# Optimization experiments

Hardware: AMD Instinct MI355X
Metric: run time of the kernel (lower is better)

Reference implementation:

```python
import jax, jax.numpy as jnp
import numpy as np

EMBED, ACT, DETER, STOCH, HID = 1536, 10, 2048, 64, 1024
T, B = 64, 256
LN_EPS = 1e-3


def _ln(x, s, b):
    mu = jnp.mean(x, axis=-1, keepdims=True)
    var = jnp.mean(jnp.square(x - mu), axis=-1, keepdims=True)
    return (x - mu) * jax.lax.rsqrt(var + LN_EPS) * s + b


def setup_inputs() -> dict:
    key = jax.random.key(0)
    ks = jax.random.split(key, 20)
    g = lambda k, shp, fan: jax.random.normal(k, shp, jnp.float32) * (1.0 / np.sqrt(fan))
    inp = {
        "embeds": jax.random.normal(ks[0], (T, B, EMBED), jnp.float32),
        "actions": jax.random.normal(ks[1], (T, B, ACT), jnp.float32),
        "h_t": jnp.zeros((B, DETER), jnp.float32),
        "z_t": jnp.zeros((B, STOCH), jnp.float32),
        "noise": jax.random.normal(ks[2], (T, B, STOCH), jnp.float32),
        # DeterNext
        "z_mlp_w": g(ks[3], (HID // 2, STOCH), STOCH),
        "z_mlp_b": jnp.zeros((HID // 2,), jnp.float32),
        "a_mlp_w": g(ks[4], (HID // 2, ACT), ACT),  # bias=False
        "ln_za_s": jnp.ones((HID,), jnp.float32),
        "ln_za_b": jnp.zeros((HID,), jnp.float32),
        # GRUCell (torch layout: [3*deter, in])
        "gru_wih": g(ks[5], (3 * DETER, HID), HID),
        "gru_whh": g(ks[6], (3 * DETER, DETER), DETER),
        "gru_bih": jnp.zeros((3 * DETER,), jnp.float32),
        "gru_bhh": jnp.zeros((3 * DETER,), jnp.float32),
        # PosteriorNext
        "post_h_w": g(ks[7], (HID, DETER), DETER),
        "post_h_b": jnp.zeros((HID,), jnp.float32),
        "post_e_w": g(ks[8], (HID, EMBED), EMBED),
        "post_e_b": jnp.zeros((HID,), jnp.float32),
        "ln_post_s": jnp.ones((HID,), jnp.float32),
        "ln_post_b": jnp.zeros((HID,), jnp.float32),
        "post_w": g(ks[9], (2 * STOCH, HID), HID),
        "post_b": jnp.zeros((2 * STOCH,), jnp.float32),
        # PriorNext
        "prior_h_w": g(ks[10], (HID, DETER), DETER),
        "prior_h_b": jnp.zeros((HID,), jnp.float32),
        "ln_prior_s": jnp.ones((HID,), jnp.float32),
        "ln_prior_b": jnp.zeros((HID,), jnp.float32),
        "prior_w": g(ks[11], (2 * STOCH, HID), HID),
        "prior_b": jnp.zeros((2 * STOCH,), jnp.float32),
    }
    return inp


def _rssm_forward(embeds, actions, h0, z0, noise,
                  z_mlp_w, z_mlp_b, a_mlp_w, ln_za_s, ln_za_b,
                  gru_wih, gru_whh, gru_bih, gru_bhh,
                  post_h_w, post_h_b, post_e_w, post_e_b, ln_post_s, ln_post_b,
                  post_w, post_b,
                  prior_h_w, prior_h_b, ln_prior_s, ln_prior_b, prior_w, prior_b):
    def step(carry, xs):
        h, z = carry
        e, a, n = xs
        # DeterNext: concat(z_mlp(z), a_mlp(a)) -> LN -> ELU
        x = jnp.concatenate([z @ z_mlp_w.T + z_mlp_b, a @ a_mlp_w.T], axis=-1)
        za = jax.nn.elu(_ln(x, ln_za_s, ln_za_b))
        # GRUCell
        gi = za @ gru_wih.T + gru_bih
        gh = h @ gru_whh.T + gru_bhh
        ir, iu, ic = jnp.split(gi, 3, axis=-1)
        hr, hu, hc = jnp.split(gh, 3, axis=-1)
        r = jax.nn.sigmoid(ir + hr)
        u = jax.nn.sigmoid(iu + hu)
        c = jnp.tanh(ic + r * hc)
        h1 = (1.0 - u) * c + u * h
        # PosteriorNext
        p = jax.nn.elu(_ln(h1 @ post_h_w.T + post_h_b + e @ post_e_w.T + post_e_b,
                           ln_post_s, ln_post_b))
        post = p @ post_w.T + post_b  # [B, 2*stoch]
        mean, sraw = jnp.split(post, 2, axis=-1)
        std = 2.0 * jax.nn.sigmoid(sraw) + 0.1
        z1 = mean + std * n  # rsample with externally-supplied noise
        return (h1, z1), (post, h1, z1)

    (_, _), (posts, states_h, post_z_samples) = jax.lax.scan(
        step, (h0, z0), (embeds, actions, noise))
    # batch prior over all timesteps
    pr = jax.nn.elu(_ln(states_h @ prior_h_w.T + prior_h_b, ln_prior_s, ln_prior_b))
    priors = pr @ prior_w.T + prior_b  # [T, B, 2*stoch]
    features = jnp.concatenate([states_h, post_z_samples], axis=-1)  # [T,B,deter+stoch]
    return priors, posts, post_z_samples, features


def reference(embeds, actions, h_t, z_t, noise,
              z_mlp_w, z_mlp_b, a_mlp_w, ln_za_s, ln_za_b,
              gru_wih, gru_whh, gru_bih, gru_bhh,
              post_h_w, post_h_b, post_e_w, post_e_b, ln_post_s, ln_post_b,
              post_w, post_b,
              prior_h_w, prior_h_b, ln_prior_s, ln_prior_b, prior_w, prior_b):
    return _rssm_forward(embeds, actions, h_t, z_t, noise,
                         z_mlp_w, z_mlp_b, a_mlp_w, ln_za_s, ln_za_b,
                         gru_wih, gru_whh, gru_bih, gru_bhh,
                         post_h_w, post_h_b, post_e_w, post_e_b, ln_post_s, ln_post_b,
                         post_w, post_b,
                         prior_h_w, prior_h_b, ln_prior_s, ln_prior_b, prior_w, prior_b)
```

## Files before the change

kernel.cpp:

```cpp
#include <hip/hip_runtime.h>

#define LN_EPS 1e-3f

typedef short s8v __attribute__((ext_vector_type(8)));
typedef float f4v __attribute__((ext_vector_type(4)));
typedef unsigned short u16;

__device__ __forceinline__ u16 f2bf(float f) {
  unsigned int x = __float_as_uint(f);
  x += 0x7fffu + ((x >> 16) & 1u);
  return (u16)(x >> 16);
}
__device__ __forceinline__ float bf2f(u16 u) {
  return __uint_as_float(((unsigned int)u) << 16);
}

__device__ __forceinline__ void glds16(const u16* g, void* l) {
  __builtin_amdgcn_global_load_lds(
      (const __attribute__((address_space(1))) void*)g,
      (__attribute__((address_space(3))) void*)l, 16, 0, 0);
}

__global__ void k_cvt(const float* __restrict__ src, u16* __restrict__ dst, int n) {
  int i = blockIdx.x * blockDim.x + threadIdx.x;
  int stride = gridDim.x * blockDim.x;
  for (; i < n; i += stride) dst[i] = f2bf(src[i]);
}

__global__ void k_packgru(const float* __restrict__ wih,
                          const float* __restrict__ whh, u16* __restrict__ wt) {
  int u = blockIdx.x * 256 + threadIdx.x;
  int nt = u / 73728;
  int r1 = u % 73728;
  int s = r1 / 1536;
  int r2 = r1 % 1536;
  int sub = r2 / 512;
  int r3 = r2 % 512;
  int ch = r3 / 64;
  int row = r3 % 64;
  int j = nt * 64 + row;
  int kbase = s * 64 + ch * 8;
  s8v v;
#pragma unroll
  for (int e = 0; e < 8; ++e) {
    int kk = kbase + e;
    float x;
    if (sub == 0) {
      x = kk < 1024 ? wih[(size_t)j * 1024 + kk] : whh[(size_t)j * 2048 + kk - 1024];
    } else if (sub == 1) {
      int jj = 2048 + j;
      x = kk < 1024 ? wih[(size_t)jj * 1024 + kk] : whh[(size_t)jj * 2048 + kk - 1024];
    } else {
      int jj = 4096 + j;
      x = (s < 16) ? wih[(size_t)jj * 1024 + kk] : whh[(size_t)jj * 2048 + kk - 1024];
    }
    v[e] = (short)f2bf(x);
  }
  *(s8v*)(wt + (size_t)u * 8) = v;
}

__global__ void k_packB(const float* __restrict__ src, u16* __restrict__ dst,
                        int K, int BN, int total) {
  int u = blockIdx.x * 256 + threadIdx.x;
  if (u >= total) return;
  int ns = K >> 6;
  int perNt = ns * 8 * BN;
  int nt = u / perNt;
  int r1 = u % perNt;
  int s = r1 / (8 * BN);
  int r2 = r1 % (8 * BN);
  int ch = r2 / BN;
  int row = r2 % BN;
  int j = nt * BN + row;
  int k = s * 64 + ch * 8;
  const float* sp = src + (size_t)j * K + k;
  s8v v;
#pragma unroll
  for (int e = 0; e < 8; ++e) v[e] = (short)f2bf(sp[e]);
  *(s8v*)(dst + (size_t)u * 8) = v;
}

__global__ void k_hinit(const float* __restrict__ h0, float* __restrict__ hf,
                        u16* __restrict__ acat) {
  int i = blockIdx.x * 256 + threadIdx.x;
  int b = i >> 11, j = i & 2047;
  float v = h0[i];
  hf[i] = v;
  acat[(size_t)b * 3072 + 1024 + j] = f2bf(v);
}

__global__ __launch_bounds__(256) void k_za(
    const float* __restrict__ zsrc, const float* __restrict__ act,
    const float* __restrict__ zw, const float* __restrict__ zb,
    const float* __restrict__ aw, const float* __restrict__ lns,
    const float* __restrict__ lnb, u16* __restrict__ acat) {
  const int b = blockIdx.x, tid = threadIdx.x;
  __shared__ float zsh[64];
  __shared__ float ash[12];
  __shared__ float wred[8];
  if (tid < 64) zsh[tid] = zsrc[b * 64 + tid];
  if (tid < 10) ash[tid] = act[b * 10 + tid];
  __syncthreads();
  float x[4];
#pragma unroll
  for (int i = 0; i < 2; ++i) {
    int c = tid + i * 256;
    const float4* wp = (const float4*)(zw + c * 64);
    float a = zb[c];
#pragma unroll
    for (int k = 0; k < 16; ++k) {
      float4 v = wp[k];
      a += zsh[k * 4] * v.x + zsh[k * 4 + 1] * v.y + zsh[k * 4 + 2] * v.z +
           zsh[k * 4 + 3] * v.w;
    }
    x[i] = a;
  }
#pragma unroll
  for (int i = 2; i < 4; ++i) {
    int c2 = tid + (i - 2) * 256;
    const float* wp = aw + c2 * 10;
    float a = 0.f;
#pragma unroll
    for (int k = 0; k < 10; ++k) a += ash[k] * wp[k];
    x[i] = a;
  }
  float s = x[0] + x[1] + x[2] + x[3];
#pragma unroll
  for (int o = 1; o < 64; o <<= 1) s += __shfl_xor(s, o);
  if ((tid & 63) == 0) wred[tid >> 6] = s;
  __syncthreads();
  float mu = (wred[0] + wred[1] + wred[2] + wred[3]) * (1.f / 1024.f);
  float q = 0.f;
#pragma unroll
  for (int i = 0; i < 4; ++i) {
    float d = x[i] - mu;
    q += d * d;
  }
#pragma unroll
  for (int o = 1; o < 64; o <<= 1) q += __shfl_xor(q, o);
  if ((tid & 63) == 0) wred[4 + (tid >> 6)] = q;
  __syncthreads();
  float rs = rsqrtf((wred[4] + wred[5] + wred[6] + wred[7]) * (1.f / 1024.f) + LN_EPS);
  int cols[4] = {tid, tid + 256, 512 + tid, 768 + tid};
#pragma unroll
  for (int i = 0; i < 4; ++i) {
    int c = cols[i];
    float y = (x[i] - mu) * rs * lns[c] + lnb[c];
    y = y > 0.f ? y : expm1f(y);
    acat[(size_t)b * 3072 + c] = f2bf(y);
  }
}

__global__ __launch_bounds__(256) void k_gru(
    const u16* __restrict__ acat_r, const u16* __restrict__ wt,
    const float* __restrict__ bih, const float* __restrict__ bhh,
    const float* __restrict__ hf_r, float* __restrict__ hf_w,
    u16* __restrict__ acat_w, float* __restrict__ feat, int t) {
  const int hw = blockIdx.x;
  const int logical = (hw & 7) * 32 + (hw >> 3);
  const int mg = logical & 7;
  const int nt = logical >> 3;
  const int m0 = mg * 32;
  const int tid = threadIdx.x;
  const int lane = tid & 63;
  const int w = tid >> 6;
  const int lr = lane & 15, lk = lane >> 4;

  __shared__ __align__(16) char smem[2][28672];

  const int arow = 8 * w + (lane >> 3);
  const int acol8 = ((lane & 7) ^ (arow & 7)) * 8;
  const u16* aSrc = acat_r + (size_t)(m0 + arow) * 3072 + acol8;
  const u16* wtNt = wt + (size_t)nt * 48 * 3 * 4096;

  f4v accr[2], accu[2], acci[2], acch[2];
  accr[0] = accr[1] = accu[0] = accu[1] = (f4v)(0.f);
  acci[0] = acci[1] = acch[0] = acch[1] = (f4v)(0.f);

#define K1_STAGE(BB, S) { \
    char* base = &smem[BB][0]; \
    glds16(aSrc + (S) * 64, base + w * 1024); \
    const u16* bsrc = wtNt + (size_t)(S) * 3 * 4096; \
    _Pragma("unroll") for (int i = 0; i < 6; ++i) { \
      int cf = w + i * 4; \
      glds16(bsrc + (cf * 64 + lane) * 8, base + 4096 + cf * 1024); \
    } }

#define K1_COMP(BB, ACCX) { \
    char* base = &smem[BB][0]; \
    _Pragma("unroll") for (int kk = 0; kk < 2; ++kk) { \
      int ch = kk * 4 + lk; \
      int r0 = lr, r1 = 16 + lr; \
      s8v a0 = *(const s8v*)(base + r0 * 128 + ((ch ^ (r0 & 7)) * 16)); \
      s8v a1 = *(const s8v*)(base + r1 * 128 + ((ch ^ (r1 & 7)) * 16)); \
      int rb = (w * 16 + lr) * 16; \
      s8v br = *(const s8v*)(base + 4096 + ch * 1024 + rb); \
      s8v bu = *(const s8v*)(base + 12288 + ch * 1024 + rb); \
      s8v bx = *(const s8v*)(base + 20480 + ch * 1024 + rb); \
      accr[0] = __builtin_amdgcn_mfma_f32_16x16x32_bf16(a0, br, accr[0], 0, 0, 0); \
      accr[1] = __builtin_amdgcn_mfma_f32_16x16x32_bf16(a1, br, accr[1], 0, 0, 0); \
      accu[0] = __builtin_amdgcn_mfma_f32_16x16x32_bf16(a0, bu, accu[0], 0, 0, 0); \
      accu[1] = __builtin_amdgcn_mfma_f32_16x16x32_bf16(a1, bu, accu[1], 0, 0, 0); \
      ACCX[0] = __builtin_amdgcn_mfma_f32_16x16x32_bf16(a0, bx, ACCX[0], 0, 0, 0); \
      ACCX[1] = __builtin_amdgcn_mfma_f32_16x16x32_bf16(a1, bx, ACCX[1], 0, 0, 0); \
    } }

  K1_STAGE(0, 0)
  int buf = 0;
  for (int s = 0; s < 16; ++s) {
    asm volatile("s_waitcnt vmcnt(0)" ::: "memory");
    __builtin_amdgcn_s_barrier();
    __builtin_amdgcn_sched_barrier(0);
    K1_STAGE(buf ^ 1, s + 1)
    K1_COMP(buf, acci)
    buf ^= 1;
  }
  for (int s = 16; s < 48; ++s) {
    asm volatile("s_waitcnt vmcnt(0)" ::: "memory");
    __builtin_amdgcn_s_barrier();
    __builtin_amdgcn_sched_barrier(0);
    if (s + 1 < 48) K1_STAGE(buf ^ 1, s + 1)
    K1_COMP(buf, acch)
    buf ^= 1;
  }

  const int j = nt * 64 + w * 16 + lr;
  const float b_ri = bih[j], b_rh = bhh[j];
  const float b_ui = bih[2048 + j], b_uh = bhh[2048 + j];
  const float b_ci = bih[4096 + j], b_ch = bhh[4096 + j];
#pragma unroll
  for (int m = 0; m < 2; ++m) {
#pragma unroll
    for (int r = 0; r < 4; ++r) {
      int grow = m0 + m * 16 + lk * 4 + r;
      float vr = accr[m][r] + b_ri + b_rh;
      float vu = accu[m][r] + b_ui + b_uh;
      float ic = acci[m][r] + b_ci;
      float hc = acch[m][r] + b_ch;
      float rg = 1.f / (1.f + expf(-vr));
      float ug = 1.f / (1.f + expf(-vu));
      float c = tanhf(ic + rg * hc);
      float hold = hf_r[(size_t)grow * 2048 + j];
      float h1 = (1.f - ug) * c + ug * hold;
      hf_w[(size_t)grow * 2048 + j] = h1;
      acat_w[(size_t)grow * 3072 + 1024 + j] = f2bf(h1);
      feat[(size_t)(t * 256 + grow) * 2112 + j] = h1;
    }
  }
#undef K1_STAGE
#undef K1_COMP
}

__global__ __launch_bounds__(256) void k_post(
    const u16* __restrict__ acat_h, const u16* __restrict__ wp,
    const float* __restrict__ bias, const u16* __restrict__ epart_t,
    float* __restrict__ xbuf) {
  const int bx = blockIdx.x;
  const int mg = bx & 7, nt = bx >> 3;
  const int m0 = mg * 32;
  const int tid = threadIdx.x;
  const int lane = tid & 63;
  const int w = tid >> 6;
  const int lr = lane & 15, lk = lane >> 4;

  __shared__ __align__(16) char smem[2][12288];

  const int arow = 8 * w + (lane >> 3);
  const int acol8 = ((lane & 7) ^ (arow & 7)) * 8;
  const u16* aSrc = acat_h + (size_t)(m0 + arow) * 3072 + 1024 + acol8;
  const u16* wpNt = wp + (size_t)nt * 32 * 4096;

  f4v acc[2];
  acc[0] = (f4v)(0.f);
  acc[1] = (f4v)(0.f);

#define K2_STAGE(BB, S) { \
    char* base = &smem[BB][0]; \
    glds16(aSrc + (S) * 64, base + w * 1024); \
    const u16* bsrc = wpNt + (size_t)(S) * 4096; \
    _Pragma("unroll") for (int i = 0; i < 2; ++i) { \
      int cf = w + i * 4; \
      glds16(bsrc + (cf * 64 + lane) * 8, base + 4096 + cf * 1024); \
    } }

  K2_STAGE(0, 0)
  int buf = 0;
  for (int s = 0; s < 32; ++s) {
    asm volatile("s_waitcnt vmcnt(0)" ::: "memory");
    __builtin_amdgcn_s_barrier();
    __builtin_amdgcn_sched_barrier(0);
    if (s + 1 < 32) K2_STAGE(buf ^ 1, s + 1)
    char* base = &smem[buf][0];
#pragma unroll
    for (int kk = 0; kk < 2; ++kk) {
      int ch = kk * 4 + lk;
      int r0 = lr, r1 = 16 + lr;
      s8v a0 = *(const s8v*)(base + r0 * 128 + ((ch ^ (r0 & 7)) * 16));
      s8v a1 = *(const s8v*)(base + r1 * 128 + ((ch ^ (r1 & 7)) * 16));
      s8v b = *(const s8v*)(base + 4096 + ch * 1024 + (w * 16 + lr) * 16);
      acc[0] = __builtin_amdgcn_mfma_f32_16x16x32_bf16(a0, b, acc[0], 0, 0, 0);
      acc[1] = __builtin_amdgcn_mfma_f32_16x16x32_bf16(a1, b, acc[1], 0, 0, 0);
    }
    buf ^= 1;
  }
  const int col = nt * 64 + w * 16 + lr;
#pragma unroll
  for (int m = 0; m < 2; ++m) {
#pragma unroll
    for (int r = 0; r < 4; ++r) {
      int grow = m0 + m * 16 + lk * 4 + r;
      float v = acc[m][r] + bias[col] + bf2f(epart_t[(size_t)grow * 1024 + col]);
      xbuf[(size_t)grow * 1024 + col] = v;
    }
  }
#undef K2_STAGE
}

__global__ __launch_bounds__(512) void k_postz(
    const float* __restrict__ xb, const u16* __restrict__ pw,
    const float* __restrict__ lns, const float* __restrict__ lnb,
    const float* __restrict__ pb, float* __restrict__ posts_t,
    const float* __restrict__ noise_t, float* __restrict__ zout,
    float* __restrict__ feat, int t) {
  const int m0 = blockIdx.x * 32;
  const int tid = threadIdx.x;
  const int lane = tid & 63;
  const int w = tid >> 6;
  const int lr = lane & 15, lk = lane >> 4;
  __shared__ __align__(16) u16 As[2][32][64];
  __shared__ __align__(16) u16 Bs[2][8][128][8];
  __shared__ float lmu[32], lrs[32];
  __shared__ float ps[32][132];
  {
    int row = tid >> 4, sg = tid & 15;
    const float4* xp = (const float4*)(xb + (size_t)(m0 + row) * 1024 + sg * 64);
    float s = 0.f, q = 0.f;
#pragma unroll
    for (int i = 0; i < 16; ++i) {
      float4 v = xp[i];
      s += v.x + v.y + v.z + v.w;
      q += v.x * v.x + v.y * v.y + v.z * v.z + v.w * v.w;
    }
#pragma unroll
    for (int o = 1; o < 16; o <<= 1) {
      s += __shfl_xor(s, o);
      q += __shfl_xor(q, o);
    }
    if (sg == 0) {
      float mu = s * (1.f / 1024.f);
      lmu[row] = mu;
      lrs[row] = rsqrtf(q * (1.f / 1024.f) - mu * mu + LN_EPS);
    }
  }
  __syncthreads();

#define K3_STAGEA(BB, S) if (tid < 256) { \
    int row = tid >> 3, k8 = tid & 7; \
    const float* xp = xb + (size_t)(m0 + row) * 1024 + (S) * 64 + k8 * 8; \
    float mu = lmu[row], rs = lrs[row]; \
    s8v v; \
    _Pragma("unroll") for (int e = 0; e < 8; ++e) { \
      int c = (S) * 64 + k8 * 8 + e; \
      float y = (xp[e] - mu) * rs * lns[c] + lnb[c]; \
      y = y > 0.f ? y : expm1f(y); \
      v[e] = (short)f2bf(y); \
    } \
    *(s8v*)((char*)&As[BB][0][0] + row * 128 + ((k8 ^ (row & 7)) * 16)) = v; }

#define K3_STAGEB(BB, S) { \
    const u16* bsrc = pw + (size_t)(S) * 8192; \
    glds16(bsrc + (((w >> 1) * 128 + (w & 1) * 64 + lane) * 8), \
           (char*)&Bs[BB][0][0][0] + w * 1024); \
    glds16(bsrc + ((((w >> 1) + 4) * 128 + (w & 1) * 64 + lane) * 8), \
           (char*)&Bs[BB][0][0][0] + w * 1024 + 8192); }

  f4v acc[2];
  acc[0] = (f4v)(0.f);
  acc[1] = (f4v)(0.f);
  K3_STAGEA(0, 0)
  K3_STAGEB(0, 0)
  __syncthreads();
  int buf = 0;
  for (int s = 0; s < 16; ++s) {
    if (s + 1 < 16) {
      K3_STAGEA(buf ^ 1, s + 1)
      K3_STAGEB(buf ^ 1, s + 1)
    }
#pragma unroll
    for (int kk = 0; kk < 2; ++kk) {
      int ch = kk * 4 + lk;
      int r0 = lr, r1 = 16 + lr;
      s8v a0 = *(const s8v*)((char*)&As[buf][0][0] + r0 * 128 + ((ch ^ (r0 & 7)) * 16));
      s8v a1 = *(const s8v*)((char*)&As[buf][0][0] + r1 * 128 + ((ch ^ (r1 & 7)) * 16));
      s8v b = *(const s8v*)((char*)&Bs[buf][0][0][0] + ch * 2048 + (w * 16 + lr) * 16);
      acc[0] = __builtin_amdgcn_mfma_f32_16x16x32_bf16(a0, b, acc[0], 0, 0, 0);
      acc[1] = __builtin_amdgcn_mfma_f32_16x16x32_bf16(a1, b, acc[1], 0, 0, 0);
    }
    __syncthreads();
    buf ^= 1;
  }
#pragma unroll
  for (int m = 0; m < 2; ++m) {
#pragma unroll
    for (int r = 0; r < 4; ++r) {
      int row = m * 16 + lk * 4 + r;
      int col = w * 16 + lr;
      float v = acc[m][r] + pb[col];
      posts_t[(size_t)(m0 + row) * 128 + col] = v;
      ps[row][col] = v;
    }
  }
  __syncthreads();
#pragma unroll
  for (int q = 0; q < 4; ++q) {
    int e = q * 512 + tid;
    int row = e >> 6, j = e & 63;
    float mean = ps[row][j], sraw = ps[row][64 + j];
    float sd = 2.f / (1.f + expf(-sraw)) + 0.1f;
    float z = mean + sd * noise_t[(m0 + row) * 64 + j];
    zout[(m0 + row) * 64 + j] = z;
    feat[(size_t)(t * 256 + m0 + row) * 2112 + 2048 + j] = z;
  }
#undef K3_STAGEA
#undef K3_STAGEB
}

template <bool AF32, bool OUTBF16>
__global__ __launch_bounds__(512) void k_gemm8(
    const void* __restrict__ Av, int lda, const u16* __restrict__ Bw, int ldb,
    int nstage, float* __restrict__ Cf, u16* __restrict__ Cb, int ldc,
    const float* __restrict__ bias) {
  const int bx = blockIdx.x, by = blockIdx.y;
  const int tid = threadIdx.x;
  const int m0 = bx * 64;
  const int n0 = by * 128;
  __shared__ __align__(16) u16 As[64][72];
  __shared__ __align__(16) u16 Bs[128][72];
  const int lane = tid & 63;
  const int w = tid >> 6;
  const int wr = w >> 2;
  const int wc = w & 3;
  const int lr = lane & 15;
  const int lk = lane >> 4;

  f4v acc[2][2];
#pragma unroll
  for (int m = 0; m < 2; ++m)
#pragma unroll
    for (int n = 0; n < 2; ++n) acc[m][n] = (f4v)(0.0f);

  for (int s = 0; s < nstage; ++s) {
    const int k0 = s << 6;
    {
      int row = tid >> 3, k8 = (tid & 7) << 3;
      if (AF32) {
        const float* ap = (const float*)Av + (size_t)(m0 + row) * lda + k0 + k8;
        float4 f0 = *(const float4*)ap;
        float4 f1 = *(const float4*)(ap + 4);
        s8v v;
        v[0] = (short)f2bf(f0.x); v[1] = (short)f2bf(f0.y);
        v[2] = (short)f2bf(f0.z); v[3] = (short)f2bf(f0.w);
        v[4] = (short)f2bf(f1.x); v[5] = (short)f2bf(f1.y);
        v[6] = (short)f2bf(f1.z); v[7] = (short)f2bf(f1.w);
        *(s8v*)&As[row][k8] = v;
      } else {
        *(s8v*)&As[row][k8] =
            *(const s8v*)((const u16*)Av + (size_t)(m0 + row) * lda + k0 + k8);
      }
    }
#pragma unroll
    for (int it = 0; it < 2; ++it) {
      int c = tid + it * 512;
      int row = c >> 3, k8 = (c & 7) << 3;
      *(s8v*)&Bs[row][k8] = *(const s8v*)(Bw + (size_t)(n0 + row) * ldb + k0 + k8);
    }
    __syncthreads();
#pragma unroll
    for (int kk = 0; kk < 2; ++kk) {
      const int koff = kk * 32 + lk * 8;
      s8v a[2], b[2];
      a[0] = *(const s8v*)&As[wr * 32 + lr][koff];
      a[1] = *(const s8v*)&As[wr * 32 + 16 + lr][koff];
      b[0] = *(const s8v*)&Bs[wc * 32 + lr][koff];
      b[1] = *(const s8v*)&Bs[wc * 32 + 16 + lr][koff];
#pragma unroll
      for (int m = 0; m < 2; ++m)
#pragma unroll
        for (int n = 0; n < 2; ++n)
          acc[m][n] =
              __builtin_amdgcn_mfma_f32_16x16x32_bf16(a[m], b[n], acc[m][n], 0, 0, 0);
    }
    __syncthreads();
  }
#pragma unroll
  for (int m = 0; m < 2; ++m) {
#pragma unroll
    for (int n = 0; n < 2; ++n) {
#pragma unroll
      for (int r = 0; r < 4; ++r) {
        int row = m0 + wr * 32 + m * 16 + lk * 4 + r;
        int col = n0 + wc * 32 + n * 16 + lr;
        float v = acc[m][n][r];
        if (bias) v += bias[col];
        if (OUTBF16)
          Cb[(size_t)row * ldc + col] = f2bf(v);
        else
          Cf[(size_t)row * ldc + col] = v;
      }
    }
  }
}

__global__ __launch_bounds__(256) void k_lnelu(const u16* __restrict__ xsrc,
                                               const float* __restrict__ s,
                                               const float* __restrict__ bb,
                                               u16* __restrict__ out) {
  int row = blockIdx.x, tid = threadIdx.x;
  __shared__ float red[256];
  float v[4];
#pragma unroll
  for (int i = 0; i < 4; ++i) {
    size_t idx = (size_t)row * 1024 + tid + i * 256;
    v[i] = bf2f(xsrc[idx]);
  }
  float sm = v[0] + v[1] + v[2] + v[3];
  red[tid] = sm;
  __syncthreads();
  for (int o = 128; o > 0; o >>= 1) {
    if (tid < o) red[tid] += red[tid + o];
    __syncthreads();
  }
  float mu = red[0] * (1.0f / 1024.0f);
  __syncthreads();
  float q = 0.f;
#pragma unroll
  for (int i = 0; i < 4; ++i) {
    float d = v[i] - mu;
    q += d * d;
  }
  red[tid] = q;
  __syncthreads();
  for (int o = 128; o > 0; o >>= 1) {
    if (tid < o) red[tid] += red[tid + o];
    __syncthreads();
  }
  float rs = rsqrtf(red[0] * (1.0f / 1024.0f) + LN_EPS);
#pragma unroll
  for (int i = 0; i < 4; ++i) {
    int c = tid + i * 256;
    float y = (v[i] - mu) * rs * s[c] + bb[c];
    y = y > 0.f ? y : expm1f(y);
    out[(size_t)row * 1024 + c] = f2bf(y);
  }
}

extern "C" void kernel_launch(void* const* d_in, const int* in_sizes, int n_in,
                              void* d_out, int out_size, void* d_ws,
                              size_t ws_size, hipStream_t stream) {
  const float* embeds = (const float*)d_in[0];
  const float* actions = (const float*)d_in[1];
  const float* h_t = (const float*)d_in[2];
  const float* z_t = (const float*)d_in[3];
  const float* noise = (const float*)d_in[4];
  const float* z_mlp_w = (const float*)d_in[5];
  const float* z_mlp_b = (const float*)d_in[6];
  const float* a_mlp_w = (const float*)d_in[7];
  const float* ln_za_s = (const float*)d_in[8];
  const float* ln_za_b = (const float*)d_in[9];
  const float* gru_wih = (const float*)d_in[10];
  const float* gru_whh = (const float*)d_in[11];
  const float* gru_bih = (const float*)d_in[12];
  const float* gru_bhh = (const float*)d_in[13];
  const float* post_h_w = (const float*)d_in[14];
  const float* post_h_b = (const float*)d_in[15];
  const float* post_e_w = (const float*)d_in[16];
  const float* post_e_b = (const float*)d_in[17];
  const float* ln_post_s = (const float*)d_in[18];
  const float* ln_post_b = (const float*)d_in[19];
  const float* post_w = (const float*)d_in[20];
  const float* post_b = (const float*)d_in[21];
  const float* prior_h_w = (const float*)d_in[22];
  const float* prior_h_b = (const float*)d_in[23];
  const float* ln_prior_s = (const float*)d_in[24];
  const float* ln_prior_b = (const float*)d_in[25];
  const float* prior_w = (const float*)d_in[26];
  const float* prior_b = (const float*)d_in[27];

  float* out = (float*)d_out;
  float* out_priors = out;
  float* out_posts = out + 2097152;
  float* out_z = out + 4194304;
  float* out_feat = out + 5242880;

  char* ws = (char*)d_ws;
  size_t off = 0;
  auto alloc = [&](size_t bytes) {
    char* p = ws + off;
    off += (bytes + 255) & ~(size_t)255;
    return p;
  };
  char* regW = alloc((size_t)32 * 48 * 3 * 4096 * 2);
  u16* wt = (u16*)regW;
  u16* prx_b = (u16*)regW;
  u16* posthP = (u16*)alloc((size_t)1024 * 2048 * 2);
  u16* postwP = (u16*)alloc((size_t)128 * 1024 * 2);
  u16* poste_b = (u16*)alloc((size_t)1024 * 1536 * 2);
  u16* priorh_b = (u16*)alloc((size_t)1024 * 2048 * 2);
  u16* priorw_b = (u16*)alloc((size_t)128 * 1024 * 2);
  u16* acat0 = (u16*)alloc((size_t)256 * 3072 * 2);
  u16* acat1 = (u16*)alloc((size_t)256 * 3072 * 2);
  float* hf0 = (float*)alloc((size_t)256 * 2048 * 4);
  float* hf1 = (float*)alloc((size_t)256 * 2048 * 4);
  float* xbuf = (float*)alloc((size_t)256 * 1024 * 4);
  char* regU = alloc((size_t)16384 * 1024 * 2);
  u16* e_part = (u16*)regU;
  u16* p_pr = (u16*)regU;

  u16* acat[2] = {acat0, acat1};
  float* hf[2] = {hf0, hf1};

  k_packgru<<<9216, 256, 0, stream>>>(gru_wih, gru_whh, wt);
  k_packB<<<1024, 256, 0, stream>>>(post_h_w, posthP, 2048, 64, 262144);
  k_packB<<<64, 256, 0, stream>>>(post_w, postwP, 1024, 128, 16384);
  k_cvt<<<512, 256, 0, stream>>>(post_e_w, poste_b, 1024 * 1536);
  k_cvt<<<512, 256, 0, stream>>>(prior_h_w, priorh_b, 1024 * 2048);
  k_cvt<<<64, 256, 0, stream>>>(prior_w, priorw_b, 128 * 1024);
  k_hinit<<<2048, 256, 0, stream>>>(h_t, hf0, acat0);

  k_gemm8<true, true><<<dim3(256, 8), 512, 0, stream>>>(
      embeds, 1536, poste_b, 1536, 24, nullptr, e_part, 1024, post_e_b);

  for (int t = 0; t < 64; ++t) {
    const int rI = t & 1, wI = rI ^ 1;
    const float* zsrc = (t == 0) ? z_t : (out_z + (size_t)(t - 1) * 16384);
    k_za<<<256, 256, 0, stream>>>(zsrc, actions + (size_t)t * 2560, z_mlp_w,
                                  z_mlp_b, a_mlp_w, ln_za_s, ln_za_b, acat[rI]);
    k_gru<<<256, 256, 0, stream>>>(acat[rI], wt, gru_bih, gru_bhh, hf[rI],
                                   hf[wI], acat[wI], out_feat, t);
    k_post<<<128, 256, 0, stream>>>(acat[wI], posthP, post_h_b,
                                    e_part + (size_t)t * 262144, xbuf);
    k_postz<<<8, 512, 0, stream>>>(xbuf, postwP, ln_post_s, ln_post_b, post_b,
                                   out_posts + (size_t)t * 32768,
                                   noise + (size_t)t * 16384,
                                   out_z + (size_t)t * 16384, out_feat, t);
  }

  k_gemm8<true, true><<<dim3(256, 8), 512, 0, stream>>>(
      out_feat, 2112, priorh_b, 2048, 32, nullptr, prx_b, 1024, prior_h_b);
  k_lnelu<<<16384, 256, 0, stream>>>(prx_b, ln_prior_s, ln_prior_b, p_pr);
  k_gemm8<false, false><<<dim3(256, 1), 512, 0, stream>>>(
      p_pr, 1024, priorw_b, 1024, 16, out_priors, nullptr, 128, prior_b);
}
```

Before: 7.119 ms.

## Fuse next-step z/action MLP into postz and retile GRU with triple buffering

Moves the per-step z/action MLP plus layernorm into the tail of k_postz, where it runs on the next timestep's action, so one launch per step disappears. The z MLP runs on MFMA using packed weights, and the action weights are pre-transposed. The GRU kernel now uses 512-thread blocks with 64-row tiles on a 128-block grid, and a 3-stage async load pipeline with partial vmcnt waits. k_post and k_postz get the same prefetch-before-wait pipelining; the tradeoffs are a large LDS footprint in postz, fewer GRU blocks, and extra serial work on only 8 blocks.

```diff
diff --git a/kernel.cpp b/kernel.cpp
--- a/kernel.cpp
+++ b/kernel.cpp
@@ -5,6 +5,8 @@
 typedef short s8v __attribute__((ext_vector_type(8)));
 typedef float f4v __attribute__((ext_vector_type(4)));
 typedef unsigned short u16;
+
+#define MFMA16 __builtin_amdgcn_mfma_f32_16x16x32_bf16
 
 __device__ __forceinline__ u16 f2bf(float f) {
   unsigned int x = __float_as_uint(f);
@@ -20,6 +22,8 @@
       (const __attribute__((address_space(1))) void*)g,
       (__attribute__((address_space(3))) void*)l, 16, 0, 0);
 }
+
+#define RAW_BAR() do { __builtin_amdgcn_s_barrier(); __builtin_amdgcn_sched_barrier(0); } while (0)
 
 __global__ void k_cvt(const float* __restrict__ src, u16* __restrict__ dst, int n) {
   int i = blockIdx.x * blockDim.x + threadIdx.x;
@@ -80,20 +84,26 @@
   *(s8v*)(dst + (size_t)u * 8) = v;
 }
 
+__global__ void k_trA(const float* __restrict__ aw, float* __restrict__ awT) {
+  int i = blockIdx.x * 256 + threadIdx.x;
+  if (i >= 5120) return;
+  int k = i >> 9, c = i & 511;
+  awT[i] = aw[c * 10 + k];
+}
+
 __global__ void k_hinit(const float* __restrict__ h0, float* __restrict__ hf,
-                        u16* __restrict__ acat) {
+                        u16* __restrict__ hcat) {
   int i = blockIdx.x * 256 + threadIdx.x;
-  int b = i >> 11, j = i & 2047;
   float v = h0[i];
   hf[i] = v;
-  acat[(size_t)b * 3072 + 1024 + j] = f2bf(v);
-}
-
-__global__ __launch_bounds__(256) void k_za(
+  hcat[i] = f2bf(v);
+}
+
+__global__ __launch_bounds__(256) void k_za0(
     const float* __restrict__ zsrc, const float* __restrict__ act,
     const float* __restrict__ zw, const float* __restrict__ zb,
     const float* __restrict__ aw, const float* __restrict__ lns,
-    const float* __restrict__ lnb, u16* __restrict__ acat) {
+    const float* __restrict__ lnb, u16* __restrict__ za) {
   const int b = blockIdx.x, tid = threadIdx.x;
   __shared__ float zsh[64];
   __shared__ float ash[12];
@@ -147,127 +157,128 @@
     int c = cols[i];
     float y = (x[i] - mu) * rs * lns[c] + lnb[c];
     y = y > 0.f ? y : expm1f(y);
-    acat[(size_t)b * 3072 + c] = f2bf(y);
-  }
-}
-
-__global__ __launch_bounds__(256) void k_gru(
-    const u16* __restrict__ acat_r, const u16* __restrict__ wt,
-    const float* __restrict__ bih, const float* __restrict__ bhh,
-    const float* __restrict__ hf_r, float* __restrict__ hf_w,
-    u16* __restrict__ acat_w, float* __restrict__ feat, int t) {
+    za[(size_t)b * 1024 + c] = f2bf(y);
+  }
+}
+
+__global__ __launch_bounds__(512) void k_gru(
+    const u16* __restrict__ za, const u16* __restrict__ hcat_r,
+    const u16* __restrict__ wt, const float* __restrict__ bih,
+    const float* __restrict__ bhh, const float* __restrict__ hf_r,
+    float* __restrict__ hf_w, u16* __restrict__ hcat_w,
+    float* __restrict__ feat, int t) {
   const int hw = blockIdx.x;
-  const int logical = (hw & 7) * 32 + (hw >> 3);
-  const int mg = logical & 7;
-  const int nt = logical >> 3;
+  const int logical = (hw & 7) * 16 + (hw >> 3);
+  const int mg = logical & 3;
+  const int nt = logical >> 2;
+  const int m0 = mg * 64;
+  const int tid = threadIdx.x;
+  const int lane = tid & 63;
+  const int w = tid >> 6;
+  const int lr = lane & 15, lk = lane >> 4;
+  const int mh = w & 1, cq = w >> 1;
+
+  __shared__ __align__(16) char bufs[3][32768];
+
+  const int arow = w * 8 + (lane >> 3);
+  const int acol8 = ((lane & 7) ^ (arow & 7)) * 8;
+  const u16* aZ = za + (size_t)(m0 + arow) * 1024 + acol8;
+  const u16* aH = hcat_r + (size_t)(m0 + arow) * 2048 + acol8;
+  const u16* wtNt = wt + (size_t)nt * 48 * 12288;
+
+  f4v accr0 = (f4v)(0.f), accr1 = (f4v)(0.f);
+  f4v accu0 = (f4v)(0.f), accu1 = (f4v)(0.f);
+  f4v acci0 = (f4v)(0.f), acci1 = (f4v)(0.f);
+  f4v acch0 = (f4v)(0.f), acch1 = (f4v)(0.f);
+
+#define G_STAGE(S) { \
+    char* base = &bufs[(S) % 3][0]; \
+    const u16* ap = ((S) < 16) ? (aZ + (S) * 64) : (aH + ((S) - 16) * 64); \
+    glds16(ap, base + w * 1024); \
+    const u16* bsrc = wtNt + (size_t)(S) * 12288; \
+    _Pragma("unroll") for (int jj = 0; jj < 3; ++jj) { \
+      int c = w + jj * 8; \
+      glds16(bsrc + c * 512 + lane * 8, base + 8192 + c * 1024); \
+    } }
+
+#define G_COMP(S, X0, X1) { \
+    char* base = &bufs[(S) % 3][0]; \
+    _Pragma("unroll") for (int kk = 0; kk < 2; ++kk) { \
+      int ch = kk * 4 + lk; \
+      int r0 = mh * 32 + lr, r1 = mh * 32 + 16 + lr; \
+      s8v a0 = *(const s8v*)(base + r0 * 128 + ((ch ^ (r0 & 7)) << 4)); \
+      s8v a1 = *(const s8v*)(base + r1 * 128 + ((ch ^ (r1 & 7)) << 4)); \
+      int boff = 8192 + ch * 1024 + ((cq * 16 + lr) << 4); \
+      s8v br = *(const s8v*)(base + boff); \
+      s8v bu = *(const s8v*)(base + boff + 8192); \
+      s8v bx = *(const s8v*)(base + boff + 16384); \
+      accr0 = MFMA16(a0, br, accr0, 0, 0, 0); \
+      accr1 = MFMA16(a1, br, accr1, 0, 0, 0); \
+      accu0 = MFMA16(a0, bu, accu0, 0, 0, 0); \
+      accu1 = MFMA16(a1, bu, accu1, 0, 0, 0); \
+      X0 = MFMA16(a0, bx, X0, 0, 0, 0); \
+      X1 = MFMA16(a1, bx, X1, 0, 0, 0); \
+    } }
+
+  G_STAGE(0)
+  G_STAGE(1)
+  for (int s = 0; s < 48; ++s) {
+    if (s + 2 < 48) { G_STAGE(s + 2) }
+    if (s < 46) asm volatile("s_waitcnt vmcnt(8)" ::: "memory");
+    else if (s == 46) asm volatile("s_waitcnt vmcnt(4)" ::: "memory");
+    else asm volatile("s_waitcnt vmcnt(0)" ::: "memory");
+    RAW_BAR();
+    if (s < 16) { G_COMP(s, acci0, acci1) }
+    else { G_COMP(s, acch0, acch1) }
+    RAW_BAR();
+  }
+#undef G_STAGE
+#undef G_COMP
+
+  const int col = nt * 64 + cq * 16 + lr;
+  const float b_r = bih[col] + bhh[col];
+  const float b_u = bih[2048 + col] + bhh[2048 + col];
+  const float b_ci = bih[4096 + col];
+  const float b_ch = bhh[4096 + col];
+#define G_EPI(AR, AU, AI, AH, MO) \
+  _Pragma("unroll") for (int r = 0; r < 4; ++r) { \
+    int grow = m0 + mh * 32 + (MO) + lk * 4 + r; \
+    float vr = AR[r] + b_r; \
+    float vu = AU[r] + b_u; \
+    float ic = AI[r] + b_ci; \
+    float hc = AH[r] + b_ch; \
+    float rg = 1.f / (1.f + expf(-vr)); \
+    float ug = 1.f / (1.f + expf(-vu)); \
+    float c = tanhf(ic + rg * hc); \
+    float hold = hf_r[(size_t)grow * 2048 + col]; \
+    float h1 = (1.f - ug) * c + ug * hold; \
+    hf_w[(size_t)grow * 2048 + col] = h1; \
+    hcat_w[(size_t)grow * 2048 + col] = f2bf(h1); \
+    feat[(size_t)(t * 256 + grow) * 2112 + col] = h1; \
+  }
+  G_EPI(accr0, accu0, acci0, acch0, 0)
+  G_EPI(accr1, accu1, acci1, acch1, 16)
+#undef G_EPI
+}
+
+__global__ __launch_bounds__(256) void k_post(
+    const u16* __restrict__ hcat, const u16* __restrict__ wp,
+    const float* __restrict__ bias, const u16* __restrict__ epart_t,
+    float* __restrict__ xbuf) {
+  const int hw = blockIdx.x;
+  const int logical = (hw & 7) * 16 + (hw >> 3);
+  const int mg = logical & 7, nt = logical >> 3;
   const int m0 = mg * 32;
   const int tid = threadIdx.x;
   const int lane = tid & 63;
   const int w = tid >> 6;
   const int lr = lane & 15, lk = lane >> 4;
 
-  __shared__ __align__(16) char smem[2][28672];
+  __shared__ __align__(16) char smem[2][12288];
 
   const int arow = 8 * w + (lane >> 3);
   const int acol8 = ((lane & 7) ^ (arow & 7)) * 8;
-  const u16* aSrc = acat_r + (size_t)(m0 + arow) * 3072 + acol8;
-  const u16* wtNt = wt + (size_t)nt * 48 * 3 * 4096;
-
-  f4v accr[2], accu[2], acci[2], acch[2];
-  accr[0] = accr[1] = accu[0] = accu[1] = (f4v)(0.f);
-  acci[0] = acci[1] = acch[0] = acch[1] = (f4v)(0.f);
-
-#define K1_STAGE(BB, S) { \
-    char* base = &smem[BB][0]; \
-    glds16(aSrc + (S) * 64, base + w * 1024); \
-    const u16* bsrc = wtNt + (size_t)(S) * 3 * 4096; \
-    _Pragma("unroll") for (int i = 0; i < 6; ++i) { \
-      int cf = w + i * 4; \
-      glds16(bsrc + (cf * 64 + lane) * 8, base + 4096 + cf * 1024); \
-    } }
-
-#define K1_COMP(BB, ACCX) { \
-    char* base = &smem[BB][0]; \
-    _Pragma("unroll") for (int kk = 0; kk < 2; ++kk) { \
-      int ch = kk * 4 + lk; \
-      int r0 = lr, r1 = 16 + lr; \
-      s8v a0 = *(const s8v*)(base + r0 * 128 + ((ch ^ (r0 & 7)) * 16)); \
-      s8v a1 = *(const s8v*)(base + r1 * 128 + ((ch ^ (r1 & 7)) * 16)); \
-      int rb = (w * 16 + lr) * 16; \
-      s8v br = *(const s8v*)(base + 4096 + ch * 1024 + rb); \
-      s8v bu = *(const s8v*)(base + 12288 + ch * 1024 + rb); \
-      s8v bx = *(const s8v*)(base + 20480 + ch * 1024 + rb); \
-      accr[0] = __builtin_amdgcn_mfma_f32_16x16x32_bf16(a0, br, accr[0], 0, 0, 0); \
-      accr[1] = __builtin_amdgcn_mfma_f32_16x16x32_bf16(a1, br, accr[1], 0, 0, 0); \
-      accu[0] = __builtin_amdgcn_mfma_f32_16x16x32_bf16(a0, bu, accu[0], 0, 0, 0); \
-      accu[1] = __builtin_amdgcn_mfma_f32_16x16x32_bf16(a1, bu, accu[1], 0, 0, 0); \
-      ACCX[0] = __builtin_amdgcn_mfma_f32_16x16x32_bf16(a0, bx, ACCX[0], 0, 0, 0); \
-      ACCX[1] = __builtin_amdgcn_mfma_f32_16x16x32_bf16(a1, bx, ACCX[1], 0, 0, 0); \
-    } }
-
-  K1_STAGE(0, 0)
-  int buf = 0;
-  for (int s = 0; s < 16; ++s) {
-    asm volatile("s_waitcnt vmcnt(0)" ::: "memory");
-    __builtin_amdgcn_s_barrier();
-    __builtin_amdgcn_sched_barrier(0);
-    K1_STAGE(buf ^ 1, s + 1)
-    K1_COMP(buf, acci)
-    buf ^= 1;
-  }
-  for (int s = 16; s < 48; ++s) {
-    asm volatile("s_waitcnt vmcnt(0)" ::: "memory");
-    __builtin_amdgcn_s_barrier();
-    __builtin_amdgcn_sched_barrier(0);
-    if (s + 1 < 48) K1_STAGE(buf ^ 1, s + 1)
-    K1_COMP(buf, acch)
-    buf ^= 1;
-  }
-
-  const int j = nt * 64 + w * 16 + lr;
-  const float b_ri = bih[j], b_rh = bhh[j];
-  const float b_ui = bih[2048 + j], b_uh = bhh[2048 + j];
-  const float b_ci = bih[4096 + j], b_ch = bhh[4096 + j];
-#pragma unroll
-  for (int m = 0; m < 2; ++m) {
-#pragma unroll
-    for (int r = 0; r < 4; ++r) {
-      int grow = m0 + m * 16 + lk * 4 + r;
-      float vr = accr[m][r] + b_ri + b_rh;
-      float vu = accu[m][r] + b_ui + b_uh;
-      float ic = acci[m][r] + b_ci;
-      float hc = acch[m][r] + b_ch;
-      float rg = 1.f / (1.f + expf(-vr));
-      float ug = 1.f / (1.f + expf(-vu));
-      float c = tanhf(ic + rg * hc);
-      float hold = hf_r[(size_t)grow * 2048 + j];
-      float h1 = (1.f - ug) * c + ug * hold;
-      hf_w[(size_t)grow * 2048 + j] = h1;
-      acat_w[(size_t)grow * 3072 + 1024 + j] = f2bf(h1);
-      feat[(size_t)(t * 256 + grow) * 2112 + j] = h1;
-    }
-  }
-#undef K1_STAGE
-#undef K1_COMP
-}
-
-__global__ __launch_bounds__(256) void k_post(
-    const u16* __restrict__ acat_h, const u16* __restrict__ wp,
-    const float* __restrict__ bias, const u16* __restrict__ epart_t,
-    float* __restrict__ xbuf) {
-  const int bx = blockIdx.x;
-  const int mg = bx & 7, nt = bx >> 3;
-  const int m0 = mg * 32;
-  const int tid = threadIdx.x;
-  const int lane = tid & 63;
-  const int w = tid >> 6;
-  const int lr = lane & 15, lk = lane >> 4;
-
-  __shared__ __align__(16) char smem[2][12288];
-
-  const int arow = 8 * w + (lane >> 3);
-  const int acol8 = ((lane & 7) ^ (arow & 7)) * 8;
-  const u16* aSrc = acat_h + (size_t)(m0 + arow) * 3072 + 1024 + acol8;
+  const u16* aSrc = hcat + (size_t)(m0 + arow) * 2048 + acol8;
   const u16* wpNt = wp + (size_t)nt * 32 * 4096;
 
   f4v acc[2];
@@ -283,26 +294,33 @@
       glds16(bsrc + (cf * 64 + lane) * 8, base + 4096 + cf * 1024); \
     } }
 
+#define K2_COMP(BB) { \
+    char* base = &smem[BB][0]; \
+    _Pragma("unroll") for (int kk = 0; kk < 2; ++kk) { \
+      int ch = kk * 4 + lk; \
+      int r0 = lr, r1 = 16 + lr; \
+      s8v a0 = *(const s8v*)(base + r0 * 128 + ((ch ^ (r0 & 7)) * 16)); \
+      s8v a1 = *(const s8v*)(base + r1 * 128 + ((ch ^ (r1 & 7)) * 16)); \
+      s8v b = *(const s8v*)(base + 4096 + ch * 1024 + (w * 16 + lr) * 16); \
+      acc[0] = MFMA16(a0, b, acc[0], 0, 0, 0); \
+      acc[1] = MFMA16(a1, b, acc[1], 0, 0, 0); \
+    } }
+
   K2_STAGE(0, 0)
-  int buf = 0;
-  for (int s = 0; s < 32; ++s) {
+  for (int s = 0; s < 31; ++s) {
+    K2_STAGE((s + 1) & 1, s + 1)
+    asm volatile("s_waitcnt vmcnt(3)" ::: "memory");
+    RAW_BAR();
+    K2_COMP(s & 1)
+    RAW_BAR();
+  }
+  {
     asm volatile("s_waitcnt vmcnt(0)" ::: "memory");
-    __builtin_amdgcn_s_barrier();
-    __builtin_amdgcn_sched_barrier(0);
-    if (s + 1 < 32) K2_STAGE(buf ^ 1, s + 1)
-    char* base = &smem[buf][0];
-#pragma unroll
-    for (int kk = 0; kk < 2; ++kk) {
-      int ch = kk * 4 + lk;
-      int r0 = lr, r1 = 16 + lr;
-      s8v a0 = *(const s8v*)(base + r0 * 128 + ((ch ^ (r0 & 7)) * 16));
-      s8v a1 = *(const s8v*)(base + r1 * 128 + ((ch ^ (r1 & 7)) * 16));
-      s8v b = *(const s8v*)(base + 4096 + ch * 1024 + (w * 16 + lr) * 16);
-      acc[0] = __builtin_amdgcn_mfma_f32_16x16x32_bf16(a0, b, acc[0], 0, 0, 0);
-      acc[1] = __builtin_amdgcn_mfma_f32_16x16x32_bf16(a1, b, acc[1], 0, 0, 0);
-    }
-    buf ^= 1;
-  }
+    RAW_BAR();
+    K2_COMP(1)
+  }
+#undef K2_STAGE
+#undef K2_COMP
   const int col = nt * 64 + w * 16 + lr;
 #pragma unroll
   for (int m = 0; m < 2; ++m) {
@@ -313,7 +331,6 @@
       xbuf[(size_t)grow * 1024 + col] = v;
     }
   }
-#undef K2_STAGE
 }
 
 __global__ __launch_bounds__(512) void k_postz(
@@ -321,16 +338,26 @@
     const float* __restrict__ lns, const float* __restrict__ lnb,
     const float* __restrict__ pb, float* __restrict__ posts_t,
     const float* __restrict__ noise_t, float* __restrict__ zout,
-    float* __restrict__ feat, int t) {
+    float* __restrict__ feat, const u16* __restrict__ zwP,
+    const float* __restrict__ zbv, const float* __restrict__ awT,
+    const float* __restrict__ act_t, const float* __restrict__ lnzs,
+    const float* __restrict__ lnzb, u16* __restrict__ za_out, int t) {
   const int m0 = blockIdx.x * 32;
   const int tid = threadIdx.x;
   const int lane = tid & 63;
   const int w = tid >> 6;
   const int lr = lane & 15, lk = lane >> 4;
-  __shared__ __align__(16) u16 As[2][32][64];
-  __shared__ __align__(16) u16 Bs[2][8][128][8];
-  __shared__ float lmu[32], lrs[32];
+  __shared__ __align__(16) u16 As[2][2048];
+  __shared__ __align__(16) u16 Bs[2][8192];
   __shared__ float ps[32][132];
+  __shared__ float lmu[32], lrsd[32];
+  __shared__ __align__(16) u16 zbl[2048];
+  __shared__ float ash[320];
+  __shared__ __align__(16) char zal[65536];
+  __shared__ float zmu[32], zrsd[32];
+  __shared__ float psum[16][32], qsum[16][32];
+
+  if (tid < 320) ash[tid] = act_t[m0 * 10 + tid];
   {
     int row = tid >> 4, sg = tid & 15;
     const float4* xp = (const float4*)(xb + (size_t)(m0 + row) * 1024 + sg * 64);
@@ -349,7 +376,7 @@
     if (sg == 0) {
       float mu = s * (1.f / 1024.f);
       lmu[row] = mu;
-      lrs[row] = rsqrtf(q * (1.f / 1024.f) - mu * mu + LN_EPS);
+      lrsd[row] = rsqrtf(q * (1.f / 1024.f) - mu * mu + LN_EPS);
     }
   }
   __syncthreads();
@@ -357,7 +384,7 @@
 #define K3_STAGEA(BB, S) if (tid < 256) { \
     int row = tid >> 3, k8 = tid & 7; \
     const float* xp = xb + (size_t)(m0 + row) * 1024 + (S) * 64 + k8 * 8; \
-    float mu = lmu[row], rs = lrs[row]; \
+    float mu = lmu[row], rs = lrsd[row]; \
     s8v v; \
     _Pragma("unroll") for (int e = 0; e < 8; ++e) { \
       int c = (S) * 64 + k8 * 8 + e; \
@@ -365,49 +392,53 @@
       y = y > 0.f ? y : expm1f(y); \
       v[e] = (short)f2bf(y); \
     } \
-    *(s8v*)((char*)&As[BB][0][0] + row * 128 + ((k8 ^ (row & 7)) * 16)) = v; }
+    *(s8v*)((char*)&As[BB][0] + row * 128 + ((k8 ^ (row & 7)) * 16)) = v; }
 
 #define K3_STAGEB(BB, S) { \
     const u16* bsrc = pw + (size_t)(S) * 8192; \
-    glds16(bsrc + (((w >> 1) * 128 + (w & 1) * 64 + lane) * 8), \
-           (char*)&Bs[BB][0][0][0] + w * 1024); \
-    glds16(bsrc + ((((w >> 1) + 4) * 128 + (w & 1) * 64 + lane) * 8), \
-           (char*)&Bs[BB][0][0][0] + w * 1024 + 8192); }
-
-  f4v acc[2];
-  acc[0] = (f4v)(0.f);
-  acc[1] = (f4v)(0.f);
+    glds16(bsrc + (w * 2) * 512 + lane * 8, (char*)&Bs[BB][0] + w * 2048); \
+    glds16(bsrc + (w * 2 + 1) * 512 + lane * 8, (char*)&Bs[BB][0] + w * 2048 + 1024); }
+
+  f4v acc0 = (f4v)(0.f), acc1 = (f4v)(0.f);
   K3_STAGEA(0, 0)
   K3_STAGEB(0, 0)
-  __syncthreads();
   int buf = 0;
   for (int s = 0; s < 16; ++s) {
     if (s + 1 < 16) {
       K3_STAGEA(buf ^ 1, s + 1)
       K3_STAGEB(buf ^ 1, s + 1)
-    }
+      asm volatile("s_waitcnt vmcnt(2) lgkmcnt(0)" ::: "memory");
+    } else {
+      asm volatile("s_waitcnt vmcnt(0) lgkmcnt(0)" ::: "memory");
+    }
+    RAW_BAR();
 #pragma unroll
     for (int kk = 0; kk < 2; ++kk) {
       int ch = kk * 4 + lk;
       int r0 = lr, r1 = 16 + lr;
-      s8v a0 = *(const s8v*)((char*)&As[buf][0][0] + r0 * 128 + ((ch ^ (r0 & 7)) * 16));
-      s8v a1 = *(const s8v*)((char*)&As[buf][0][0] + r1 * 128 + ((ch ^ (r1 & 7)) * 16));
-      s8v b = *(const s8v*)((char*)&Bs[buf][0][0][0] + ch * 2048 + (w * 16 + lr) * 16);
-      acc[0] = __builtin_amdgcn_mfma_f32_16x16x32_bf16(a0, b, acc[0], 0, 0, 0);
-      acc[1] = __builtin_amdgcn_mfma_f32_16x16x32_bf16(a1, b, acc[1], 0, 0, 0);
-    }
-    __syncthreads();
+      s8v a0 = *(const s8v*)((char*)&As[buf][0] + r0 * 128 + ((ch ^ (r0 & 7)) * 16));
+      s8v a1 = *(const s8v*)((char*)&As[buf][0] + r1 * 128 + ((ch ^ (r1 & 7)) * 16));
+      s8v b = *(const s8v*)((char*)&Bs[buf][0] + ch * 2048 + (w * 16 + lr) * 16);
+      acc0 = MFMA16(a0, b, acc0, 0, 0, 0);
+      acc1 = MFMA16(a1, b, acc1, 0, 0, 0);
+    }
+    __builtin_amdgcn_s_barrier();
     buf ^= 1;
   }
-#pragma unroll
-  for (int m = 0; m < 2; ++m) {
+#undef K3_STAGEA
+#undef K3_STAGEB
+
+  {
+    int colp = w * 16 + lr;
 #pragma unroll
     for (int r = 0; r < 4; ++r) {
-      int row = m * 16 + lk * 4 + r;
-      int col = w * 16 + lr;
-      float v = acc[m][r] + pb[col];
-      posts_t[(size_t)(m0 + row) * 128 + col] = v;
-      ps[row][col] = v;
+      int row0 = lk * 4 + r;
+      float v0 = acc0[r] + pb[colp];
+      posts_t[(size_t)(m0 + row0) * 128 + colp] = v0;
+      ps[row0][colp] = v0;
+      float v1 = acc1[r] + pb[colp];
+      posts_t[(size_t)(m0 + 16 + row0) * 128 + colp] = v1;
+      ps[16 + row0][colp] = v1;
     }
   }
   __syncthreads();
@@ -420,9 +451,105 @@
     float z = mean + sd * noise_t[(m0 + row) * 64 + j];
     zout[(m0 + row) * 64 + j] = z;
     feat[(size_t)(t * 256 + m0 + row) * 2112 + 2048 + j] = z;
-  }
-#undef K3_STAGEA
-#undef K3_STAGEB
+    *(u16*)((char*)&zbl[0] + row * 128 + (((j >> 3) ^ (row & 7)) << 4) +
+            (j & 7) * 2) = f2bf(z);
+  }
+  __syncthreads();
+
+  {
+    float acc[32];
+#pragma unroll
+    for (int r = 0; r < 32; ++r) acc[r] = 0.f;
+#pragma unroll
+    for (int k = 0; k < 10; ++k) {
+      float wv = awT[k * 512 + tid];
+#pragma unroll
+      for (int r = 0; r < 32; ++r) acc[r] += ash[r * 10 + k] * wv;
+    }
+    int c = 512 + tid;
+    int chs = c >> 3, cb = (c & 7) * 2;
+#pragma unroll
+    for (int r = 0; r < 32; ++r)
+      *(u16*)(zal + r * 2048 + ((chs ^ (r & 7)) << 4) + cb) = f2bf(acc[r]);
+  }
+  for (int c4 = 0; c4 < 4; ++c4) {
+    glds16(zwP + c4 * 8192 + (w * 2) * 512 + lane * 8, (char*)&Bs[0][0] + w * 2048);
+    glds16(zwP + c4 * 8192 + (w * 2 + 1) * 512 + lane * 8,
+           (char*)&Bs[0][0] + w * 2048 + 1024);
+    asm volatile("s_waitcnt vmcnt(0)" ::: "memory");
+    RAW_BAR();
+    f4v z0 = (f4v)(0.f), z1 = (f4v)(0.f);
+#pragma unroll
+    for (int kk = 0; kk < 2; ++kk) {
+      int ch = kk * 4 + lk;
+      int r0 = lr, r1 = 16 + lr;
+      s8v a0 = *(const s8v*)((char*)&zbl[0] + r0 * 128 + ((ch ^ (r0 & 7)) << 4));
+      s8v a1 = *(const s8v*)((char*)&zbl[0] + r1 * 128 + ((ch ^ (r1 & 7)) << 4));
+      s8v b = *(const s8v*)((char*)&Bs[0][0] + ch * 2048 + (w * 16 + lr) * 16);
+      z0 = MFMA16(a0, b, z0, 0, 0, 0);
+      z1 = MFMA16(a1, b, z1, 0, 0, 0);
+    }
+    int zcol = c4 * 128 + w * 16 + lr;
+    int chz = zcol >> 3, cbz = (zcol & 7) * 2;
+    float zbias = zbv[zcol];
+#pragma unroll
+    for (int r = 0; r < 4; ++r) {
+      int ra = lk * 4 + r, rb = 16 + lk * 4 + r;
+      *(u16*)(zal + ra * 2048 + ((chz ^ (ra & 7)) << 4) + cbz) = f2bf(z0[r] + zbias);
+      *(u16*)(zal + rb * 2048 + ((chz ^ (rb & 7)) << 4) + cbz) = f2bf(z1[r] + zbias);
+    }
+    RAW_BAR();
+  }
+  __syncthreads();
+  {
+    int row = tid & 31, g = tid >> 5;
+    float s = 0.f, q = 0.f;
+#pragma unroll
+    for (int jj = 0; jj < 8; ++jj) {
+      int chunk = g * 8 + jj;
+      s8v v = *(const s8v*)(zal + row * 2048 + ((chunk ^ (row & 7)) << 4));
+#pragma unroll
+      for (int e = 0; e < 8; ++e) {
+        float x = bf2f((u16)v[e]);
+        s += x;
+        q += x * x;
+      }
+    }
+    psum[g][row] = s;
+    qsum[g][row] = q;
+    __syncthreads();
+    if (tid < 32) {
+      float ss = 0.f, qq = 0.f;
+#pragma unroll
+      for (int gg = 0; gg < 16; ++gg) {
+        ss += psum[gg][tid];
+        qq += qsum[gg][tid];
+      }
+      float mu = ss * (1.f / 1024.f);
+      zmu[tid] = mu;
+      zrsd[tid] = rsqrtf(qq * (1.f / 1024.f) - mu * mu + LN_EPS);
+    }
+  }
+  __syncthreads();
+  {
+    int row = tid >> 4, g = tid & 15;
+    float mu = zmu[row], rs = zrsd[row];
+    u16* dst = za_out + (size_t)(m0 + row) * 1024 + g * 64;
+#pragma unroll
+    for (int jj = 0; jj < 8; ++jj) {
+      int chunk = g * 8 + jj;
+      s8v v = *(const s8v*)(zal + row * 2048 + ((chunk ^ (row & 7)) << 4));
+      s8v o;
+#pragma unroll
+      for (int e = 0; e < 8; ++e) {
+        int c = chunk * 8 + e;
+        float y = (bf2f((u16)v[e]) - mu) * rs * lnzs[c] + lnzb[c];
+        y = y > 0.f ? y : expm1f(y);
+        o[e] = (short)f2bf(y);
+      }
+      *(s8v*)(dst + jj * 8) = o;
+    }
+  }
 }
 
 template <bool AF32, bool OUTBF16>
@@ -487,8 +614,7 @@
       for (int m = 0; m < 2; ++m)
 #pragma unroll
         for (int n = 0; n < 2; ++n)
-          acc[m][n] =
-              __builtin_amdgcn_mfma_f32_16x16x32_bf16(a[m], b[n], acc[m][n], 0, 0, 0);
+          acc[m][n] = MFMA16(a[m], b[n], acc[m][n], 0, 0, 0);
     }
     __syncthreads();
   }
@@ -599,7 +725,7 @@
     off += (bytes + 255) & ~(size_t)255;
     return p;
   };
-  char* regW = alloc((size_t)32 * 48 * 3 * 4096 * 2);
+  char* regW = alloc((size_t)32 * 48 * 12288 * 2);
   u16* wt = (u16*)regW;
   u16* prx_b = (u16*)regW;
   u16* posthP = (u16*)alloc((size_t)1024 * 2048 * 2);
@@ -607,42 +733,48 @@
   u16* poste_b = (u16*)alloc((size_t)1024 * 1536 * 2);
   u16* priorh_b = (u16*)alloc((size_t)1024 * 2048 * 2);
   u16* priorw_b = (u16*)alloc((size_t)128 * 1024 * 2);
-  u16* acat0 = (u16*)alloc((size_t)256 * 3072 * 2);
-  u16* acat1 = (u16*)alloc((size_t)256 * 3072 * 2);
+  u16* zwP = (u16*)alloc((size_t)512 * 64 * 2);
+  float* awT = (float*)alloc((size_t)10 * 512 * 4);
+  u16* hcat0 = (u16*)alloc((size_t)256 * 2048 * 2);
+  u16* hcat1 = (u16*)alloc((size_t)256 * 2048 * 2);
   float* hf0 = (float*)alloc((size_t)256 * 2048 * 4);
   float* hf1 = (float*)alloc((size_t)256 * 2048 * 4);
   float* xbuf = (float*)alloc((size_t)256 * 1024 * 4);
+  u16* za = (u16*)alloc((size_t)256 * 1024 * 2);
   char* regU = alloc((size_t)16384 * 1024 * 2);
   u16* e_part = (u16*)regU;
   u16* p_pr = (u16*)regU;
 
-  u16* acat[2] = {acat0, acat1};
+  u16* hcat[2] = {hcat0, hcat1};
   float* hf[2] = {hf0, hf1};
 
   k_packgru<<<9216, 256, 0, stream>>>(gru_wih, gru_whh, wt);
   k_packB<<<1024, 256, 0, stream>>>(post_h_w, posthP, 2048, 64, 262144);
   k_packB<<<64, 256, 0, stream>>>(post_w, postwP, 1024, 128, 16384);
+  k_packB<<<16, 256, 0, stream>>>(z_mlp_w, zwP, 64, 128, 4096);
+  k_trA<<<20, 256, 0, stream>>>(a_mlp_w, awT);
   k_cvt<<<512, 256, 0, stream>>>(post_e_w, poste_b, 1024 * 1536);
   k_cvt<<<512, 256, 0, stream>>>(prior_h_w, priorh_b, 1024 * 2048);
   k_cvt<<<64, 256, 0, stream>>>(prior_w, priorw_b, 128 * 1024);
-  k_hinit<<<2048, 256, 0, stream>>>(h_t, hf0, acat0);
+  k_hinit<<<2048, 256, 0, stream>>>(h_t, hf0, hcat0);
+  k_za0<<<256, 256, 0, stream>>>(z_t, actions, z_mlp_w, z_mlp_b, a_mlp_w,
+                                 ln_za_s, ln_za_b, za);
 
   k_gemm8<true, true><<<dim3(256, 8), 512, 0, stream>>>(
       embeds, 1536, poste_b, 1536, 24, nullptr, e_part, 1024, post_e_b);
 
   for (int t = 0; t < 64; ++t) {
     const int rI = t & 1, wI = rI ^ 1;
-    const float* zsrc = (t == 0) ? z_t : (out_z + (size_t)(t - 1) * 16384);
-    k_za<<<256, 256, 0, stream>>>(zsrc, actions + (size_t)t * 2560, z_mlp_w,
-                                  z_mlp_b, a_mlp_w, ln_za_s, ln_za_b, acat[rI]);
-    k_gru<<<256, 256, 0, stream>>>(acat[rI], wt, gru_bih, gru_bhh, hf[rI],
-                                   hf[wI], acat[wI], out_feat, t);
-    k_post<<<128, 256, 0, stream>>>(acat[wI], posthP, post_h_b,
+    k_gru<<<128, 512, 0, stream>>>(za, hcat[rI], wt, gru_bih, gru_bhh, hf[rI],
+                                   hf[wI], hcat[wI], out_feat, t);
+    k_post<<<128, 256, 0, stream>>>(hcat[wI], posthP, post_h_b,
                                     e_part + (size_t)t * 262144, xbuf);
-    k_postz<<<8, 512, 0, stream>>>(xbuf, postwP, ln_post_s, ln_post_b, post_b,
-                                   out_posts + (size_t)t * 32768,
-                                   noise + (size_t)t * 16384,
-                                   out_z + (size_t)t * 16384, out_feat, t);
+    k_postz<<<8, 512, 0, stream>>>(
+        xbuf, postwP, ln_post_s, ln_post_b, post_b,
+        out_posts + (size_t)t * 32768, noise + (size_t)t * 16384,
+        out_z + (size_t)t * 16384, out_feat, zwP, z_mlp_b, awT,
+        actions + (size_t)(t + 1 < 64 ? t + 1 : t) * 2560, ln_za_s, ln_za_b,
+        za, t);
   }
 
   k_gemm8<true, true><<<dim3(256, 8), 512, 0, stream>>>(
```

Result: slower. 8.619 ms (+21.1%).
